# Performance work log

Measured on AMD Instinct MI355X. Metric: run time of the kernel, lower is better.

Reference implementation:

```python
import jax, jax.numpy as jnp
import numpy as np

N_NODES = 1024
CHANNELS = [1, 64, 128]
DENSE = [196608, 256]
SAMPLE_NUMBER = 50


def _glorot(key, shape):
    fan_in, fan_out = shape[0], shape[-1]
    s = jnp.sqrt(6.0 / (fan_in + fan_out))
    return jax.random.uniform(key, shape, jnp.float32, -s, s)


def setup_inputs() -> dict:
    key = jax.random.key(0)
    ks = jax.random.split(key, 20)
    T, B = 16, 64
    inp = {
        "xs_seq": jax.random.normal(ks[0], (T, B, N_NODES, CHANNELS[0]), jnp.float32),
        "adj": jax.random.uniform(ks[1], (N_NODES, N_NODES), jnp.float32) / N_NODES,
    }
    # GCGRU params per layer: gates z, r, candidate n over concat([x, h])
    ki = 2
    for li in range(len(CHANNELS) - 1):
        cin, cout = CHANNELS[li], CHANNELS[li + 1]
        for g in ("z", "r", "n"):
            inp[f"W{g}{li}"] = _glorot(ks[ki], (cin + cout, cout)); ki += 1
            inp[f"b{g}{li}"] = jnp.zeros((cout,), jnp.float32)
    inp["W_mu"] = _glorot(ks[ki], (DENSE[0], DENSE[1])); ki += 1
    inp["b_mu"] = jnp.zeros((DENSE[1],), jnp.float32)
    inp["W_lv"] = _glorot(ks[ki], (DENSE[0], DENSE[1])); ki += 1
    inp["b_lv"] = jnp.zeros((DENSE[1],), jnp.float32)
    return inp


def _gcgru(xs, adj, Wz, bz, Wr, br, Wn, bn, cout):
    # xs: [T, B, N, cin]; graph-conv GRU over time via scan
    T, B, N, _ = xs.shape
    h0 = jnp.zeros((B, N, cout), xs.dtype)

    def gconv(a, x, W, b):  # adj @ x @ W + b
        return jnp.einsum("ij,bjc,cd->bid", a, x, W) + b

    def step(h, x):
        xh = jnp.concatenate([x, h], axis=-1)
        z = jax.nn.sigmoid(gconv(adj, xh, Wz, bz))
        r = jax.nn.sigmoid(gconv(adj, xh, Wr, br))
        xrh = jnp.concatenate([x, r * h], axis=-1)
        n = jnp.tanh(gconv(adj, xrh, Wn, bn))
        h_new = (1.0 - z) * h + z * n
        return h_new, h_new

    _, hs = jax.lax.scan(step, h0, xs)
    return hs  # [T, B, N, cout]


def _forward(xs_seq, adj, Wz0, bz0, Wr0, br0, Wn0, bn0,
             Wz1, bz1, Wr1, br1, Wn1, bn1, W_mu, b_mu, W_lv, b_lv, eps):
    h1 = _gcgru(xs_seq, adj, Wz0, bz0, Wr0, br0, Wn0, bn0, CHANNELS[1])
    h2 = _gcgru(h1, adj, Wz1, bz1, Wr1, br1, Wn1, bn1, CHANNELS[2])
    xs = jnp.concatenate([h1[-1], h2[-1]], axis=2)  # [B, N, C1+C2]
    B = xs.shape[0]
    xs = xs.reshape(B, -1)  # [B, N*(C1+C2)]
    mu = jax.nn.sigmoid(xs @ W_mu + b_mu)
    logvar = jax.nn.sigmoid(xs @ W_lv + b_lv)
    std = jnp.exp(0.5 * logvar)
    z = mu + eps * std
    return z, mu, logvar


def reference(xs_seq, adj, Wz0, bz0, Wr0, br0, Wn0, bn0,
              Wz1, bz1, Wr1, br1, Wn1, bn1, W_mu, b_mu, W_lv, b_lv):
    B = xs_seq.shape[1]
    ekey = jax.random.fold_in(jax.random.key(0), 1234)
    eps = jax.random.normal(ekey, (SAMPLE_NUMBER, B, DENSE[1]), jnp.float32).mean(0)
    return _forward(xs_seq, adj, Wz0, bz0, Wr0, br0, Wn0, bn0,
                    Wz1, bz1, Wr1, br1, Wn1, bn1, W_mu, b_mu, W_lv, b_lv, eps)
```

## Files before the change

### kernel.cpp

```cpp
#include <hip/hip_runtime.h>
#include <math.h>

#define EPS_MODE 0

typedef unsigned short u16;
typedef short bf16x8 __attribute__((ext_vector_type(8)));
typedef float f32x4 __attribute__((ext_vector_type(4)));
typedef u16 u16x4 __attribute__((ext_vector_type(4)));
typedef u16 u16x8 __attribute__((ext_vector_type(8)));

static constexpr int T = 16;
static constexpr size_t MF = 1u << 20;
static constexpr int DKCH = 256;
static constexpr int DKCHUNK = 196608 / DKCH;

__device__ __forceinline__ u16 f2bf(float f) {
  unsigned u = __float_as_uint(f);
  unsigned r = (u + 0x7fffu + ((u >> 16) & 1u)) >> 16;
  return (u16)r;
}
__device__ __forceinline__ float bf2f(u16 h) {
  return __uint_as_float(((unsigned)h) << 16);
}
__device__ __forceinline__ void gload16(const void* g, void* l) {
  __builtin_amdgcn_global_load_lds(
      (const __attribute__((address_space(1))) void*)g,
      (__attribute__((address_space(3))) void*)l, 16, 0, 0);
}

__global__ __launch_bounds__(256) void cast_bf16(const float* __restrict__ in,
                                                 u16* __restrict__ out, int n) {
  int i = (blockIdx.x * 256 + threadIdx.x) * 4;
  if (i < n) {
    float4 v = *reinterpret_cast<const float4*>(&in[i]);
    out[i + 0] = f2bf(v.x); out[i + 1] = f2bf(v.y);
    out[i + 2] = f2bf(v.z); out[i + 3] = f2bf(v.w);
  }
}

__global__ __launch_bounds__(256) void prep_wt(const float* __restrict__ Wz0, const float* __restrict__ Wr0,
                                               const float* __restrict__ Wn0, const float* __restrict__ Wz1,
                                               const float* __restrict__ Wr1, const float* __restrict__ Wn1,
                                               u16* __restrict__ WzrT0, u16* __restrict__ WnT0,
                                               u16* __restrict__ WzrT1, u16* __restrict__ WnT1) {
  int seg = blockIdx.y;
  int idx = blockIdx.x * 256 + threadIdx.x;
  if (seg == 0) {
    if (idx < 128 * 64) {
      int j = idx >> 6, k = idx & 63;
      float v = (j < 64) ? Wz0[(k + 1) * 64 + j] : Wr0[(k + 1) * 64 + (j - 64)];
      WzrT0[idx] = f2bf(v);
    }
  } else if (seg == 1) {
    if (idx < 64 * 64) {
      int j = idx >> 6, k = idx & 63;
      WnT0[idx] = f2bf(Wn0[(k + 1) * 64 + j]);
    }
  } else if (seg == 2) {
    if (idx < 256 * 192) {
      int j = idx / 192, k = idx % 192;
      float v = (j < 128) ? Wz1[k * 128 + j] : Wr1[k * 128 + (j - 128)];
      WzrT1[idx] = f2bf(v);
    }
  } else {
    if (idx < 128 * 192) {
      int j = idx / 192, k = idx % 192;
      WnT1[idx] = f2bf(Wn1[k * 128 + j]);
    }
  }
}

template <int EPI, int LOGC, int MFR>
__global__ __launch_bounds__(256) void adj_mfma(const u16* __restrict__ A,
                                                const u16* __restrict__ BT,
                                                void* __restrict__ OUT) {
  constexpr int MT = MFR * 32;
  __shared__ __align__(16) char lds[(MFR + 4) * 4096];
  int tid = threadIdx.x;
  int w = tid >> 6, lane = tid & 63;
  int row0 = blockIdx.y * MT, col0 = blockIdx.x * 128;
  int wm = w >> 1, wn = w & 1;
  f32x4 acc[MFR][4] = {};
  for (int k0 = 0; k0 < 1024; k0 += 64) {
#pragma unroll
    for (int q = 0; q < MFR; ++q) {
      int row = q * 32 + w * 8 + (lane >> 3);
      gload16(A + (size_t)(row0 + row) * 1024 + k0 + (lane & 7) * 8,
              lds + q * 4096 + w * 1024);
    }
#pragma unroll
    for (int q = 0; q < 4; ++q) {
      int row = q * 32 + w * 8 + (lane >> 3);
      gload16(BT + (size_t)(col0 + row) * 1024 + k0 + (lane & 7) * 8,
              lds + MFR * 4096 + q * 4096 + w * 1024);
    }
    __syncthreads();
#pragma unroll
    for (int kk = 0; kk < 2; ++kk) {
      bf16x8 a[MFR], bb[4];
#pragma unroll
      for (int m = 0; m < MFR; ++m)
        a[m] = *(const bf16x8*)(lds + (wm * (MFR * 16) + m * 16 + (lane & 15)) * 128 + kk * 64 + (lane >> 4) * 16);
#pragma unroll
      for (int n = 0; n < 4; ++n)
        bb[n] = *(const bf16x8*)(lds + MFR * 4096 + (wn * 64 + n * 16 + (lane & 15)) * 128 + kk * 64 + (lane >> 4) * 16);
#pragma unroll
      for (int m = 0; m < MFR; ++m)
#pragma unroll
        for (int n = 0; n < 4; ++n)
          acc[m][n] = __builtin_amdgcn_mfma_f32_16x16x32_bf16(a[m], bb[n], acc[m][n], 0, 0, 0);
    }
    __syncthreads();
  }
  if (EPI == 1) {
    float* O = (float*)OUT;
#pragma unroll
    for (int m = 0; m < MFR; ++m)
#pragma unroll
      for (int n = 0; n < 4; ++n) {
        int col = col0 + wn * 64 + n * 16 + (lane & 15);
        int t = col >> 6, bbx = col & 63;
        int row = row0 + wm * (MFR * 16) + m * 16 + ((lane >> 4) << 2);
        *(float4*)&O[((size_t)t << 16) + ((size_t)bbx << 10) + row] = *(float4*)&acc[m][n];
      }
  } else {
    u16* O = (u16*)OUT;
    constexpr int C = 1 << LOGC;
#pragma unroll
    for (int m = 0; m < MFR; ++m)
#pragma unroll
      for (int n = 0; n < 4; ++n) {
        int col = col0 + wn * 64 + n * 16 + (lane & 15);
        int bbx = col >> LOGC, c = col & (C - 1);
#pragma unroll
        for (int j = 0; j < 4; ++j) {
          int row = row0 + wm * (MFR * 16) + m * 16 + ((lane >> 4) << 2) + j;
          O[(((size_t)bbx << 10) + row) * C + c] = f2bf(acc[m][n][j]);
        }
      }
  }
}

template <int C, int RK1, int MFR>
__global__ __launch_bounds__(256) void adj_ngate(
    const u16* __restrict__ A, const u16* __restrict__ BT,
    const u16* __restrict__ WnT, const float* __restrict__ bias,
    const float* __restrict__ axv, const float* __restrict__ wx,
    const u16* __restrict__ AH1, const u16* __restrict__ zT,
    u16* __restrict__ hT) {
  constexpr int LOGC = (C == 64) ? 6 : 7;
  constexpr int KW = (C == 64) ? 64 : 192;
  constexpr int KKAN = C / 32;
  constexpr int MT = MFR * 32;
  constexpr int STG = (MFR + 4) * 4096;
  constexpr int ANBYTES = MT * 136 * 2;
  constexpr int LDSZ = STG > ANBYTES ? STG : ANBYTES;
  __shared__ __align__(16) char lds[LDSZ];
  int tid = threadIdx.x;
  int w = tid >> 6, lane = tid & 63;
  int row0 = blockIdx.y * MT, col0 = blockIdx.x * 128;
  int wm = w >> 1, wn = w & 1;
  f32x4 acc[MFR][4] = {};
  for (int k0 = 0; k0 < 1024; k0 += 64) {
#pragma unroll
    for (int q = 0; q < MFR; ++q) {
      int row = q * 32 + w * 8 + (lane >> 3);
      gload16(A + (size_t)(row0 + row) * 1024 + k0 + (lane & 7) * 8,
              lds + q * 4096 + w * 1024);
    }
#pragma unroll
    for (int q = 0; q < 4; ++q) {
      int row = q * 32 + w * 8 + (lane >> 3);
      gload16(BT + (size_t)(col0 + row) * 1024 + k0 + (lane & 7) * 8,
              lds + MFR * 4096 + q * 4096 + w * 1024);
    }
    __syncthreads();
#pragma unroll
    for (int kk = 0; kk < 2; ++kk) {
      bf16x8 a[MFR], bb[4];
#pragma unroll
      for (int m = 0; m < MFR; ++m)
        a[m] = *(const bf16x8*)(lds + (wm * (MFR * 16) + m * 16 + (lane & 15)) * 128 + kk * 64 + (lane >> 4) * 16);
#pragma unroll
      for (int n = 0; n < 4; ++n)
        bb[n] = *(const bf16x8*)(lds + MFR * 4096 + (wn * 64 + n * 16 + (lane & 15)) * 128 + kk * 64 + (lane >> 4) * 16);
#pragma unroll
      for (int m = 0; m < MFR; ++m)
#pragma unroll
        for (int n = 0; n < 4; ++n)
          acc[m][n] = __builtin_amdgcn_mfma_f32_16x16x32_bf16(a[m], bb[n], acc[m][n], 0, 0, 0);
    }
    __syncthreads();
  }
  u16* ANt = (u16*)lds;
#pragma unroll
  for (int m = 0; m < MFR; ++m)
#pragma unroll
    for (int n = 0; n < 4; ++n) {
      int cl = wn * 64 + n * 16 + (lane & 15);
      int rl = wm * (MFR * 16) + m * 16 + ((lane >> 4) << 2);
#pragma unroll
      for (int j = 0; j < 4; ++j)
        ANt[(rl + j) * 136 + cl] = f2bf(acc[m][n][j]);
    }
  __syncthreads();
  int wrow = w >> 1, half = w & 1;
  int arow0 = wrow * (MFR * 16);
  int b0 = col0 >> LOGC;
  int out0 = (C == 64) ? 0 : half * 64;
  int kbase = (C == 64) ? half * 64 : 0;
  int b_eff = (C == 64) ? (b0 + half) : b0;
  constexpr int WOFF = (C == 64) ? 0 : 64;
  f32x4 acc2[MFR][4] = {};
#pragma unroll
  for (int kk = 0; kk < KKAN; ++kk) {
    bf16x8 a[MFR], bb[4];
    int ka = kbase + kk * 32 + (lane >> 4) * 8;
#pragma unroll
    for (int m = 0; m < MFR; ++m)
      a[m] = *(const bf16x8*)&ANt[(arow0 + m * 16 + (lane & 15)) * 136 + ka];
#pragma unroll
    for (int n = 0; n < 4; ++n)
      bb[n] = *(const bf16x8*)&WnT[(size_t)(out0 + n * 16 + (lane & 15)) * KW + WOFF + kk * 32 + (lane >> 4) * 8];
#pragma unroll
    for (int m = 0; m < MFR; ++m)
#pragma unroll
      for (int n = 0; n < 4; ++n)
        acc2[m][n] = __builtin_amdgcn_mfma_f32_16x16x32_bf16(a[m], bb[n], acc2[m][n], 0, 0, 0);
  }
  if (C == 128) {
#pragma unroll
    for (int kk = 0; kk < 2; ++kk) {
      bf16x8 a[MFR], bb[4];
#pragma unroll
      for (int m = 0; m < MFR; ++m)
        a[m] = *(const bf16x8*)&AH1[(((size_t)b0 << 10) + row0 + arow0 + m * 16 + (lane & 15)) * 64 + kk * 32 + (lane >> 4) * 8];
#pragma unroll
      for (int n = 0; n < 4; ++n)
        bb[n] = *(const bf16x8*)&WnT[(size_t)(out0 + n * 16 + (lane & 15)) * 192 + kk * 32 + (lane >> 4) * 8];
#pragma unroll
      for (int m = 0; m < MFR; ++m)
#pragma unroll
        for (int n = 0; n < 4; ++n)
          acc2[m][n] = __builtin_amdgcn_mfma_f32_16x16x32_bf16(a[m], bb[n], acc2[m][n], 0, 0, 0);
    }
  }
#pragma unroll
  for (int m = 0; m < MFR; ++m) {
    float ax4[4];
    if (RK1) {
      float4 v = *(const float4*)&axv[((size_t)b_eff << 10) + row0 + arow0 + m * 16 + ((lane >> 4) << 2)];
      ax4[0] = v.x; ax4[1] = v.y; ax4[2] = v.z; ax4[3] = v.w;
    }
#pragma unroll
    for (int n = 0; n < 4; ++n) {
      int cp = out0 + n * 16 + (lane & 15);
      int grow = arow0 + m * 16 + ((lane >> 4) << 2);
      size_t idx = (((size_t)b_eff << LOGC) + cp) * 1024 + row0 + grow;
      u16x4 zv = *(const u16x4*)&zT[idx];
      u16x4 hv = *(const u16x4*)&hT[idx];
      u16x4 pk;
#pragma unroll
      for (int j = 0; j < 4; ++j) {
        float g = acc2[m][n][j] + bias[cp];
        if (RK1) g += ax4[j] * wx[cp];
        float nv = tanhf(g);
        float z = bf2f(zv[j]), ho = bf2f(hv[j]);
        pk[j] = f2bf((1.f - z) * ho + z * nv);
      }
      *(u16x4*)&hT[idx] = pk;
    }
  }
}

template <int WM, int WN, int C, int NK1, int NK, int RK1>
__global__ __launch_bounds__(256) void gate_zr(
    const u16* __restrict__ A1, const u16* __restrict__ A2,
    const u16* __restrict__ WT, const float* __restrict__ bz,
    const float* __restrict__ br, const float* __restrict__ axv,
    const float* __restrict__ wxz, const float* __restrict__ wxr,
    const u16* __restrict__ hT, u16* __restrict__ zTo, u16* __restrict__ rhTo) {
  constexpr int MT = WM * 64, NT = WN * 64, K = NK * 64;
  constexpr int NB = 1024 / MT;
  __shared__ __align__(16) char lds[MT * 128 + NT * 128];
  int tid = threadIdx.x;
  int w = tid >> 6, lane = tid & 63;
  int by = blockIdx.x;
  int b = by / NB, n0 = (by % NB) * MT;
  size_t row0 = ((size_t)b << 10) + n0;
  int wm = w / WN, wn = w % WN;
  f32x4 acc[4][4] = {};
  for (int s = 0; s < NK; ++s) {
    const u16* As; int astr, koff;
    if (s < NK1) { As = A1; astr = 64; koff = s * 64; }
    else         { As = A2; astr = 128; koff = (s - NK1) * 64; }
#pragma unroll
    for (int q = 0; q < MT / 32; ++q) {
      int row = q * 32 + w * 8 + (lane >> 3);
      gload16(As + (row0 + row) * astr + koff + (lane & 7) * 8,
              lds + q * 4096 + w * 1024);
    }
#pragma unroll
    for (int q = 0; q < NT / 32; ++q) {
      int row = q * 32 + w * 8 + (lane >> 3);
      gload16(WT + (size_t)row * K + s * 64 + (lane & 7) * 8,
              lds + MT * 128 + q * 4096 + w * 1024);
    }
    __syncthreads();
#pragma unroll
    for (int kk = 0; kk < 2; ++kk) {
      bf16x8 a[4], bb[4];
#pragma unroll
      for (int m = 0; m < 4; ++m)
        a[m] = *(const bf16x8*)(lds + (wm * 64 + m * 16 + (lane & 15)) * 128 + kk * 64 + (lane >> 4) * 16);
#pragma unroll
      for (int n = 0; n < 4; ++n)
        bb[n] = *(const bf16x8*)(lds + MT * 128 + (wn * 64 + n * 16 + (lane & 15)) * 128 + kk * 64 + (lane >> 4) * 16);
#pragma unroll
      for (int m = 0; m < 4; ++m)
#pragma unroll
        for (int n = 0; n < 4; ++n)
          acc[m][n] = __builtin_amdgcn_mfma_f32_16x16x32_bf16(a[m], bb[n], acc[m][n], 0, 0, 0);
    }
    __syncthreads();
  }
#pragma unroll
  for (int m = 0; m < 4; ++m) {
    float ax4[4];
    if (RK1) {
      float4 v = *(const float4*)&axv[row0 + wm * 64 + m * 16 + ((lane >> 4) << 2)];
      ax4[0] = v.x; ax4[1] = v.y; ax4[2] = v.z; ax4[3] = v.w;
    }
#pragma unroll
    for (int n = 0; n < 4; ++n) {
      int cp = wn * 64 + n * 16 + (lane & 15);
      bool iz = cp < C;
      int c = iz ? cp : cp - C;
      int rl = wm * 64 + m * 16 + ((lane >> 4) << 2);
      size_t idx = (((size_t)b * C + c) << 10) + n0 + rl;
      u16x4 hv;
      if (!iz) hv = *(const u16x4*)&hT[idx];
      u16x4 pk;
#pragma unroll
      for (int j = 0; j < 4; ++j) {
        float g = acc[m][n][j] + (iz ? bz : br)[c];
        if (RK1) g += ax4[j] * (iz ? wxz : wxr)[c];
        float sg = 1.f / (1.f + expf(-g));
        pk[j] = iz ? f2bf(sg) : f2bf(sg * bf2f(hv[j]));
      }
      *(u16x4*)&(iz ? zTo : rhTo)[idx] = pk;
    }
  }
}

__global__ __launch_bounds__(256) void transpose_x(const u16* __restrict__ h1T,
                                                   const u16* __restrict__ h2T,
                                                   u16* __restrict__ X) {
  int b = blockIdx.x;
  int n0 = blockIdx.y * 128;
  __shared__ u16 tile[192][136];
  int tid = threadIdx.x;
#pragma unroll
  for (int i = 0; i < 12; ++i) {
    int id = tid + i * 256;
    int c = id >> 4, g = id & 15;
    u16x8 v;
    if (c < 64) v = *(const u16x8*)&h1T[(((size_t)b << 6) + c) * 1024 + n0 + g * 8];
    else        v = *(const u16x8*)&h2T[(((size_t)b << 7) + (c - 64)) * 1024 + n0 + g * 8];
    *(u16x8*)&tile[c][g * 8] = v;
  }
  __syncthreads();
#pragma unroll
  for (int i = 0; i < 12; ++i) {
    int id = tid + i * 256;
    int n = id / 24, g = id % 24;
    u16x8 v;
#pragma unroll
    for (int j = 0; j < 8; ++j) v[j] = tile[g * 8 + j][n];
    *(u16x8*)&X[(size_t)b * 196608 + (size_t)(n0 + n) * 192 + g * 8] = v;
  }
}

__global__ __launch_bounds__(256) void dense_split(const u16* __restrict__ X,
                                                   const float* __restrict__ Wmu,
                                                   const float* __restrict__ Wlv,
                                                   float* __restrict__ P) {
  int ot = blockIdx.x, ch = blockIdx.y, mat = blockIdx.z;
  const float* W = mat ? Wlv : Wmu;
  int o0 = ot * 64;
  __shared__ float As[16][68];
  __shared__ float Ws[16][68];
  int tid = threadIdx.x;
  int tx = tid & 15, ty = tid >> 4;
  int ab = tid >> 2, akq = (tid & 3) * 4;
  int wkk = tid >> 4, wo4 = (tid & 15) * 4;
  int kb = ch * DKCHUNK;
  float acc[4][4] = {};
  u16x4 xa = *(const u16x4*)&X[(size_t)ab * 196608 + kb + akq];
  float4 wv = *(const float4*)&W[(size_t)(kb + wkk) * 256 + o0 + wo4];
  for (int s = 0; s < DKCHUNK / 16; ++s) {
#pragma unroll
    for (int j = 0; j < 4; ++j) As[akq + j][ab] = bf2f(xa[j]);
    *(float4*)&Ws[wkk][wo4] = wv;
    __syncthreads();
    if (s + 1 < DKCHUNK / 16) {
      int k0 = kb + (s + 1) * 16;
      xa = *(const u16x4*)&X[(size_t)ab * 196608 + k0 + akq];
      wv = *(const float4*)&W[(size_t)(k0 + wkk) * 256 + o0 + wo4];
    }
#pragma unroll
    for (int kk = 0; kk < 16; ++kk) {
      float a[4], bq[4];
      *(float4*)a = *(const float4*)&As[kk][ty * 4];
      *(float4*)bq = *(const float4*)&Ws[kk][tx * 4];
#pragma unroll
      for (int i = 0; i < 4; ++i)
#pragma unroll
        for (int j = 0; j < 4; ++j) acc[i][j] += a[i] * bq[j];
    }
    __syncthreads();
  }
#pragma unroll
  for (int i = 0; i < 4; ++i) {
    float4 v; v.x = acc[i][0]; v.y = acc[i][1]; v.z = acc[i][2]; v.w = acc[i][3];
    *(float4*)&P[(((size_t)mat * DKCH + ch) * 64 + ty * 4 + i) * 256 + o0 + tx * 4] = v;
  }
}

__device__ __forceinline__ unsigned rotl32(unsigned v, int s) {
  return (v << s) | (v >> (32 - s));
}
__device__ void threefry(unsigned k0, unsigned k1, unsigned x0, unsigned x1,
                         unsigned& o0, unsigned& o1) {
  unsigned ks2 = k0 ^ k1 ^ 0x1BD11BDAu;
  unsigned a = x0 + k0, b = x1 + k1;
#define TF_RND(rot) { a += b; b = rotl32(b, rot); b ^= a; }
  TF_RND(13) TF_RND(15) TF_RND(26) TF_RND(6)
  a += k1; b += ks2 + 1u;
  TF_RND(17) TF_RND(29) TF_RND(16) TF_RND(24)
  a += ks2; b += k0 + 2u;
  TF_RND(13) TF_RND(15) TF_RND(26) TF_RND(6)
  a += k0; b += k1 + 3u;
  TF_RND(17) TF_RND(29) TF_RND(16) TF_RND(24)
  a += k1; b += ks2 + 4u;
  TF_RND(13) TF_RND(15) TF_RND(26) TF_RND(6)
  a += ks2; b += k0 + 5u;
#undef TF_RND
  o0 = a; o1 = b;
}

__device__ float u32_to_normal(unsigned bits) {
  unsigned fb = (bits >> 9) | 0x3F800000u;
  float f = __uint_as_float(fb) - 1.0f;
  const float lo = -0.99999994f;
  float u = f * 2.0f + lo;
  u = fmaxf(lo, u);
  float w = -log1pf(-u * u);
  float p;
  if (w < 5.0f) {
    w -= 2.5f;
    p = 2.81022636e-08f;
    p = fmaf(p, w, 3.43273939e-07f);
    p = fmaf(p, w, -3.5233877e-06f);
    p = fmaf(p, w, -4.39150654e-06f);
    p = fmaf(p, w, 0.00021858087f);
    p = fmaf(p, w, -0.00125372503f);
    p = fmaf(p, w, -0.00417768164f);
    p = fmaf(p, w, 0.246640727f);
    p = fmaf(p, w, 1.50140941f);
  } else {
    w = sqrtf(w) - 3.0f;
    p = -0.000200214257f;
    p = fmaf(p, w, 0.000100950558f);
    p = fmaf(p, w, 0.00134934322f);
    p = fmaf(p, w, -0.00367342844f);
    p = fmaf(p, w, 0.00573950773f);
    p = fmaf(p, w, -0.0076224613f);
    p = fmaf(p, w, 0.00943887047f);
    p = fmaf(p, w, 1.00167406f);
    p = fmaf(p, w, 2.83297682f);
  }
  return 1.41421354f * (p * u);
}

__global__ __launch_bounds__(256) void eps_kernel(float* __restrict__ eps) {
  int b = blockIdx.x;
  int o = threadIdx.x;
  unsigned k0, k1;
  threefry(0u, 0u, 0u, 1234u, k0, k1);
  float s = 0.f;
  for (int smp = 0; smp < 50; ++smp) {
    unsigned idx = ((unsigned)smp * 64u + (unsigned)b) * 256u + (unsigned)o;
    unsigned o0, o1, bits;
#if EPS_MODE == 0
    threefry(k0, k1, 0u, idx, o0, o1);
    bits = o0 ^ o1;
#else
    unsigned pp = idx % 409600u, half = idx / 409600u;
    threefry(k0, k1, pp, pp + 409600u, o0, o1);
    bits = half ? o1 : o0;
#endif
    s += u32_to_normal(bits);
  }
  eps[b * 256 + o] = s / 50.0f;
}

__global__ __launch_bounds__(256) void final_kernel(const float* __restrict__ P,
                                                    const float* __restrict__ bmu,
                                                    const float* __restrict__ blv,
                                                    const float* __restrict__ eps,
                                                    float* __restrict__ out) {
  int b = blockIdx.x, o = threadIdx.x;
  float smu = 0.f, slv = 0.f;
  for (int ch = 0; ch < DKCH; ++ch) {
    smu += P[(((size_t)0 * DKCH + ch) * 64 + b) * 256 + o];
    slv += P[(((size_t)1 * DKCH + ch) * 64 + b) * 256 + o];
  }
  float mu = 1.f / (1.f + expf(-(smu + bmu[o])));
  float lv = 1.f / (1.f + expf(-(slv + blv[o])));
  float z = mu + eps[b * 256 + o] * expf(0.5f * lv);
  out[b * 256 + o] = z;
  out[16384 + b * 256 + o] = mu;
  out[32768 + b * 256 + o] = lv;
}

extern "C" void kernel_launch(void* const* d_in, const int* in_sizes, int n_in,
                              void* d_out, int out_size, void* d_ws, size_t ws_size,
                              hipStream_t stream) {
  (void)in_sizes; (void)n_in; (void)out_size; (void)ws_size;
  const float* xs  = (const float*)d_in[0];
  const float* adj = (const float*)d_in[1];
  const float* Wz0 = (const float*)d_in[2];  const float* bz0 = (const float*)d_in[3];
  const float* Wr0 = (const float*)d_in[4];  const float* br0 = (const float*)d_in[5];
  const float* Wn0 = (const float*)d_in[6];  const float* bn0 = (const float*)d_in[7];
  const float* Wz1 = (const float*)d_in[8];  const float* bz1 = (const float*)d_in[9];
  const float* Wr1 = (const float*)d_in[10]; const float* br1 = (const float*)d_in[11];
  const float* Wn1 = (const float*)d_in[12]; const float* bn1 = (const float*)d_in[13];
  const float* Wmu = (const float*)d_in[14]; const float* bmu = (const float*)d_in[15];
  const float* Wlv = (const float*)d_in[16]; const float* blv = (const float*)d_in[17];

  float* ws = (float*)d_ws;
  u16*  adjB  = (u16*)(ws);
  u16*  xsB   = (u16*)(ws + MF / 2);
  float* AXv  = ws + 1 * MF;
  u16*  h1T   = (u16*)(ws + 2 * MF);
  u16*  h2T   = (u16*)(ws + 4 * MF);
  u16*  z0T   = (u16*)(ws + 8 * MF);
  u16*  z1T   = (u16*)(ws + 10 * MF);
  u16*  rh0T  = (u16*)(ws + 14 * MF);
  u16*  rh1T  = (u16*)(ws + 16 * MF);
  u16*  AH1   = (u16*)(ws + 20 * MF);
  u16*  AH2   = (u16*)(ws + 22 * MF);
  u16*  WTb   = (u16*)(ws + 26 * MF);
  u16*  X     = (u16*)(ws + 8 * MF);
  float* P    = ws + 16 * MF;
  float* EPS  = ws + 24 * MF;

  u16* WzrT0 = WTb;
  u16* WnT0  = WTb + 8192;
  u16* WzrT1 = WTb + 12288;
  u16* WnT1  = WTb + 61440;

  hipMemsetAsync(ws + 2 * MF, 0, 6 * MF * sizeof(float), stream);
  hipMemsetAsync(ws + 20 * MF, 0, 6 * MF * sizeof(float), stream);

  cast_bf16<<<1024, 256, 0, stream>>>(adj, adjB, 1 << 20);
  cast_bf16<<<1024, 256, 0, stream>>>(xs, xsB, 1 << 20);
  prep_wt<<<dim3(192, 4), 256, 0, stream>>>(Wz0, Wr0, Wn0, Wz1, Wr1, Wn1,
                                            WzrT0, WnT0, WzrT1, WnT1);

  adj_mfma<1, 0, 4><<<dim3(8, 8), 256, 0, stream>>>(adjB, xsB, AXv);

  for (int t = 0; t < T; ++t) {
    const float* AXt = AXv + (size_t)t * 65536;
    gate_zr<2, 2, 64, 1, 1, 1><<<512, 256, 0, stream>>>(
        AH1, nullptr, WzrT0, bz0, br0, AXt, Wz0, Wr0, h1T, z0T, rh0T);
    adj_ngate<64, 1, 2><<<dim3(32, 16), 256, 0, stream>>>(
        adjB, rh0T, WnT0, bn0, AXt, Wn0, nullptr, z0T, h1T);
    adj_mfma<0, 6, 2><<<dim3(32, 16), 256, 0, stream>>>(adjB, h1T, AH1);
    gate_zr<1, 4, 128, 1, 3, 0><<<1024, 256, 0, stream>>>(
        AH1, AH2, WzrT1, bz1, br1, nullptr, nullptr, nullptr, h2T, z1T, rh1T);
    adj_ngate<128, 0, 4><<<dim3(64, 8), 256, 0, stream>>>(
        adjB, rh1T, WnT1, bn1, nullptr, nullptr, AH1, z1T, h2T);
    if (t + 1 < T)
      adj_mfma<0, 7, 4><<<dim3(64, 8), 256, 0, stream>>>(adjB, h2T, AH2);
  }

  transpose_x<<<dim3(64, 8), 256, 0, stream>>>(h1T, h2T, X);
  dense_split<<<dim3(4, DKCH, 2), 256, 0, stream>>>(X, Wmu, Wlv, P);
  eps_kernel<<<64, 256, 0, stream>>>(EPS);
  final_kernel<<<64, 256, 0, stream>>>(P, bmu, blv, EPS, (float*)d_out);
}
```

Measured before the change: 3.025 ms.

## Skew GRU layers in time and fuse both layers' stages into combined kernels

Refactors the gate, n-gate and adjacency-matmul kernels into device functions. The time loop is then software-pipelined: layer-0 step t+1 runs in the same launch as layer-1 step t, through three combined kernels that dispatch by block index. This halves the number of launches per timestep and fills the GPU with more blocks per launch, to cut launch and tail-latency overhead in the serial recurrence. It also raises the layer-0 adjacency row tile from 2 to 4 MFMA fragments. It adds prologue and epilogue launches, and the combined kernels carry the larger shared-memory footprint of both branches, which may lower occupancy.

New measurement: 3.125 ms. 3.3% more time.

```diff
diff --git a/kernel.cpp b/kernel.cpp
--- a/kernel.cpp
+++ b/kernel.cpp
@@ -71,14 +71,14 @@
 }
 
 template <int EPI, int LOGC, int MFR>
-__global__ __launch_bounds__(256) void adj_mfma(const u16* __restrict__ A,
-                                                const u16* __restrict__ BT,
-                                                void* __restrict__ OUT) {
+__device__ __forceinline__ void dev_adj_mfma(int bx, int by, char* lds,
+                                             const u16* __restrict__ A,
+                                             const u16* __restrict__ BT,
+                                             void* __restrict__ OUT) {
   constexpr int MT = MFR * 32;
-  __shared__ __align__(16) char lds[(MFR + 4) * 4096];
   int tid = threadIdx.x;
   int w = tid >> 6, lane = tid & 63;
-  int row0 = blockIdx.y * MT, col0 = blockIdx.x * 128;
+  int row0 = by * MT, col0 = bx * 128;
   int wm = w >> 1, wn = w & 1;
   f32x4 acc[MFR][4] = {};
   for (int k0 = 0; k0 < 1024; k0 += 64) {
@@ -141,8 +141,17 @@
   }
 }
 
+template <int EPI, int LOGC, int MFR>
+__global__ __launch_bounds__(256) void adj_mfma(const u16* __restrict__ A,
+                                                const u16* __restrict__ BT,
+                                                void* __restrict__ OUT) {
+  __shared__ __align__(16) char lds[(MFR + 4) * 4096];
+  dev_adj_mfma<EPI, LOGC, MFR>(blockIdx.x, blockIdx.y, lds, A, BT, OUT);
+}
+
 template <int C, int RK1, int MFR>
-__global__ __launch_bounds__(256) void adj_ngate(
+__device__ __forceinline__ void dev_adj_ngate(
+    int bx, int by, char* lds,
     const u16* __restrict__ A, const u16* __restrict__ BT,
     const u16* __restrict__ WnT, const float* __restrict__ bias,
     const float* __restrict__ axv, const float* __restrict__ wx,
@@ -152,13 +161,9 @@
   constexpr int KW = (C == 64) ? 64 : 192;
   constexpr int KKAN = C / 32;
   constexpr int MT = MFR * 32;
-  constexpr int STG = (MFR + 4) * 4096;
-  constexpr int ANBYTES = MT * 136 * 2;
-  constexpr int LDSZ = STG > ANBYTES ? STG : ANBYTES;
-  __shared__ __align__(16) char lds[LDSZ];
   int tid = threadIdx.x;
   int w = tid >> 6, lane = tid & 63;
-  int row0 = blockIdx.y * MT, col0 = blockIdx.x * 128;
+  int row0 = by * MT, col0 = bx * 128;
   int wm = w >> 1, wn = w & 1;
   f32x4 acc[MFR][4] = {};
   for (int k0 = 0; k0 < 1024; k0 += 64) {
@@ -273,8 +278,25 @@
   }
 }
 
+template <int C, int RK1, int MFR>
+__global__ __launch_bounds__(256) void adj_ngate(
+    const u16* __restrict__ A, const u16* __restrict__ BT,
+    const u16* __restrict__ WnT, const float* __restrict__ bias,
+    const float* __restrict__ axv, const float* __restrict__ wx,
+    const u16* __restrict__ AH1, const u16* __restrict__ zT,
+    u16* __restrict__ hT) {
+  constexpr int MT = MFR * 32;
+  constexpr int STG = (MFR + 4) * 4096;
+  constexpr int ANB = MT * 136 * 2;
+  constexpr int LDSZ = STG > ANB ? STG : ANB;
+  __shared__ __align__(16) char lds[LDSZ];
+  dev_adj_ngate<C, RK1, MFR>(blockIdx.x, blockIdx.y, lds, A, BT, WnT, bias, axv, wx,
+                             AH1, zT, hT);
+}
+
 template <int WM, int WN, int C, int NK1, int NK, int RK1>
-__global__ __launch_bounds__(256) void gate_zr(
+__device__ __forceinline__ void dev_gate_zr(
+    int by, char* lds,
     const u16* __restrict__ A1, const u16* __restrict__ A2,
     const u16* __restrict__ WT, const float* __restrict__ bz,
     const float* __restrict__ br, const float* __restrict__ axv,
@@ -282,10 +304,8 @@
     const u16* __restrict__ hT, u16* __restrict__ zTo, u16* __restrict__ rhTo) {
   constexpr int MT = WM * 64, NT = WN * 64, K = NK * 64;
   constexpr int NB = 1024 / MT;
-  __shared__ __align__(16) char lds[MT * 128 + NT * 128];
   int tid = threadIdx.x;
   int w = tid >> 6, lane = tid & 63;
-  int by = blockIdx.x;
   int b = by / NB, n0 = (by % NB) * MT;
   size_t row0 = ((size_t)b << 10) + n0;
   int wm = w / WN, wn = w % WN;
@@ -350,6 +370,67 @@
       }
       *(u16x4*)&(iz ? zTo : rhTo)[idx] = pk;
     }
+  }
+}
+
+template <int WM, int WN, int C, int NK1, int NK, int RK1>
+__global__ __launch_bounds__(256) void gate_zr(
+    const u16* __restrict__ A1, const u16* __restrict__ A2,
+    const u16* __restrict__ WT, const float* __restrict__ bz,
+    const float* __restrict__ br, const float* __restrict__ axv,
+    const float* __restrict__ wxz, const float* __restrict__ wxr,
+    const u16* __restrict__ hT, u16* __restrict__ zTo, u16* __restrict__ rhTo) {
+  __shared__ __align__(16) char lds[WM * 64 * 128 + WN * 64 * 128];
+  dev_gate_zr<WM, WN, C, NK1, NK, RK1>(blockIdx.x, lds, A1, A2, WT, bz, br, axv,
+                                       wxz, wxr, hT, zTo, rhTo);
+}
+
+__global__ __launch_bounds__(256) void combo_zr(
+    const u16* __restrict__ AH1, const u16* __restrict__ AH2,
+    const u16* __restrict__ WzrT1, const float* __restrict__ bz1, const float* __restrict__ br1,
+    const u16* __restrict__ h2T, u16* __restrict__ z1T, u16* __restrict__ rh1T,
+    const u16* __restrict__ WzrT0, const float* __restrict__ bz0, const float* __restrict__ br0,
+    const float* __restrict__ AXt1, const float* __restrict__ Wz0, const float* __restrict__ Wr0,
+    const u16* __restrict__ h1T, u16* __restrict__ z0T, u16* __restrict__ rh0T) {
+  __shared__ __align__(16) char lds[40960];
+  int bid = blockIdx.x;
+  if (bid < 1024)
+    dev_gate_zr<1, 4, 128, 1, 3, 0>(bid, lds, AH1, AH2, WzrT1, bz1, br1, nullptr,
+                                    nullptr, nullptr, h2T, z1T, rh1T);
+  else
+    dev_gate_zr<2, 2, 64, 1, 1, 1>(bid - 1024, lds, AH1, nullptr, WzrT0, bz0, br0,
+                                   AXt1, Wz0, Wr0, h1T, z0T, rh0T);
+}
+
+__global__ __launch_bounds__(256) void combo_ngate(
+    const u16* __restrict__ adjB,
+    const u16* __restrict__ rh1T, const u16* __restrict__ WnT1, const float* __restrict__ bn1,
+    const u16* __restrict__ AH1, const u16* __restrict__ z1T, u16* __restrict__ h2T,
+    const u16* __restrict__ rh0T, const u16* __restrict__ WnT0, const float* __restrict__ bn0,
+    const float* __restrict__ AXt1, const float* __restrict__ Wn0,
+    const u16* __restrict__ z0T, u16* __restrict__ h1T) {
+  __shared__ __align__(16) char lds[34816];
+  int bid = blockIdx.x;
+  if (bid < 512)
+    dev_adj_ngate<128, 0, 4>(bid & 63, bid >> 6, lds, adjB, rh1T, WnT1, bn1,
+                             nullptr, nullptr, AH1, z1T, h2T);
+  else {
+    int b2 = bid - 512;
+    dev_adj_ngate<64, 1, 4>(b2 & 31, b2 >> 5, lds, adjB, rh0T, WnT0, bn0,
+                            AXt1, Wn0, nullptr, z0T, h1T);
+  }
+}
+
+__global__ __launch_bounds__(256) void combo_ah(
+    const u16* __restrict__ adjB, const u16* __restrict__ h2T, u16* __restrict__ AH2,
+    const u16* __restrict__ h1T, u16* __restrict__ AH1) {
+  __shared__ __align__(16) char lds[32768];
+  int bid = blockIdx.x;
+  if (bid < 512)
+    dev_adj_mfma<0, 7, 4>(bid & 63, bid >> 6, lds, adjB, h2T, AH2);
+  else {
+    int b2 = bid - 512;
+    dev_adj_mfma<0, 6, 4>(b2 & 31, b2 >> 5, lds, adjB, h1T, AH1);
   }
 }
 
@@ -571,20 +652,25 @@
 
   adj_mfma<1, 0, 4><<<dim3(8, 8), 256, 0, stream>>>(adjB, xsB, AXv);
 
-  for (int t = 0; t < T; ++t) {
-    const float* AXt = AXv + (size_t)t * 65536;
-    gate_zr<2, 2, 64, 1, 1, 1><<<512, 256, 0, stream>>>(
-        AH1, nullptr, WzrT0, bz0, br0, AXt, Wz0, Wr0, h1T, z0T, rh0T);
-    adj_ngate<64, 1, 2><<<dim3(32, 16), 256, 0, stream>>>(
-        adjB, rh0T, WnT0, bn0, AXt, Wn0, nullptr, z0T, h1T);
-    adj_mfma<0, 6, 2><<<dim3(32, 16), 256, 0, stream>>>(adjB, h1T, AH1);
-    gate_zr<1, 4, 128, 1, 3, 0><<<1024, 256, 0, stream>>>(
-        AH1, AH2, WzrT1, bz1, br1, nullptr, nullptr, nullptr, h2T, z1T, rh1T);
-    adj_ngate<128, 0, 4><<<dim3(64, 8), 256, 0, stream>>>(
-        adjB, rh1T, WnT1, bn1, nullptr, nullptr, AH1, z1T, h2T);
-    if (t + 1 < T)
-      adj_mfma<0, 7, 4><<<dim3(64, 8), 256, 0, stream>>>(adjB, h2T, AH2);
-  }
+  gate_zr<2, 2, 64, 1, 1, 1><<<512, 256, 0, stream>>>(
+      AH1, nullptr, WzrT0, bz0, br0, AXv, Wz0, Wr0, h1T, z0T, rh0T);
+  adj_ngate<64, 1, 4><<<dim3(32, 8), 256, 0, stream>>>(
+      adjB, rh0T, WnT0, bn0, AXv, Wn0, nullptr, z0T, h1T);
+  adj_mfma<0, 6, 4><<<dim3(32, 8), 256, 0, stream>>>(adjB, h1T, AH1);
+
+  for (int i = 0; i < T - 1; ++i) {
+    const float* AXt1 = AXv + (size_t)(i + 1) * 65536;
+    combo_zr<<<1536, 256, 0, stream>>>(AH1, AH2, WzrT1, bz1, br1, h2T, z1T, rh1T,
+                                       WzrT0, bz0, br0, AXt1, Wz0, Wr0, h1T, z0T, rh0T);
+    combo_ngate<<<768, 256, 0, stream>>>(adjB, rh1T, WnT1, bn1, AH1, z1T, h2T,
+                                         rh0T, WnT0, bn0, AXt1, Wn0, z0T, h1T);
+    combo_ah<<<768, 256, 0, stream>>>(adjB, h2T, AH2, h1T, AH1);
+  }
+
+  gate_zr<1, 4, 128, 1, 3, 0><<<1024, 256, 0, stream>>>(
+      AH1, AH2, WzrT1, bz1, br1, nullptr, nullptr, nullptr, h2T, z1T, rh1T);
+  adj_ngate<128, 0, 4><<<dim3(64, 8), 256, 0, stream>>>(
+      adjB, rh1T, WnT1, bn1, nullptr, nullptr, AH1, z1T, h2T);
 
   transpose_x<<<dim3(64, 8), 256, 0, stream>>>(h1T, h2T, X);
   dense_split<<<dim3(4, DKCH, 2), 256, 0, stream>>>(X, Wmu, Wlv, P);
```

## Rewrite dense split-K GEMM with bf16 MFMA and retune layer-2 adj kernels

Applied to the files above, without the earlier changes.

Replaces the scalar FP32 tiled dense projection with an MFMA bf16 kernel. Each block now covers all 256 outputs of one K chunk, staging X through LDS and converting W to bf16 on the fly. The FP32 weight stream (about 400MB across both matrices) still dominates, and converting W to bf16 reduces the precision of the product. Separately, the layer-2 adj_ngate and adj_mfma launches switch to a smaller per-block tile template argument with twice as many blocks.

Result: slower. 3.239 ms (+7.1%).

```diff
diff --git a/kernel.cpp b/kernel.cpp
--- a/kernel.cpp
+++ b/kernel.cpp
@@ -381,50 +381,72 @@
   }
 }
 
-__global__ __launch_bounds__(256) void dense_split(const u16* __restrict__ X,
+__global__ __launch_bounds__(256) void dense_mfma2(const u16* __restrict__ X,
                                                    const float* __restrict__ Wmu,
                                                    const float* __restrict__ Wlv,
                                                    float* __restrict__ P) {
-  int ot = blockIdx.x, ch = blockIdx.y, mat = blockIdx.z;
+  __shared__ __align__(16) char lds[8192 + 256 * 70 * 2];
+  u16* Bs = (u16*)(lds + 8192);
+  int tid = threadIdx.x, w = tid >> 6, lane = tid & 63;
+  int ch = blockIdx.x, mat = blockIdx.y;
   const float* W = mat ? Wlv : Wmu;
-  int o0 = ot * 64;
-  __shared__ float As[16][68];
-  __shared__ float Ws[16][68];
-  int tid = threadIdx.x;
-  int tx = tid & 15, ty = tid >> 4;
-  int ab = tid >> 2, akq = (tid & 3) * 4;
-  int wkk = tid >> 4, wo4 = (tid & 15) * 4;
   int kb = ch * DKCHUNK;
-  float acc[4][4] = {};
-  u16x4 xa = *(const u16x4*)&X[(size_t)ab * 196608 + kb + akq];
-  float4 wv = *(const float4*)&W[(size_t)(kb + wkk) * 256 + o0 + wo4];
-  for (int s = 0; s < DKCHUNK / 16; ++s) {
-#pragma unroll
-    for (int j = 0; j < 4; ++j) As[akq + j][ab] = bf2f(xa[j]);
-    *(float4*)&Ws[wkk][wo4] = wv;
-    __syncthreads();
-    if (s + 1 < DKCHUNK / 16) {
-      int k0 = kb + (s + 1) * 16;
-      xa = *(const u16x4*)&X[(size_t)ab * 196608 + k0 + akq];
-      wv = *(const float4*)&W[(size_t)(k0 + wkk) * 256 + o0 + wo4];
-    }
-#pragma unroll
-    for (int kk = 0; kk < 16; ++kk) {
-      float a[4], bq[4];
-      *(float4*)a = *(const float4*)&As[kk][ty * 4];
-      *(float4*)bq = *(const float4*)&Ws[kk][tx * 4];
-#pragma unroll
-      for (int i = 0; i < 4; ++i)
-#pragma unroll
-        for (int j = 0; j < 4; ++j) acc[i][j] += a[i] * bq[j];
-    }
-    __syncthreads();
-  }
-#pragma unroll
-  for (int i = 0; i < 4; ++i) {
-    float4 v; v.x = acc[i][0]; v.y = acc[i][1]; v.z = acc[i][2]; v.w = acc[i][3];
-    *(float4*)&P[(((size_t)mat * DKCH + ch) * 64 + ty * 4 + i) * 256 + o0 + tx * 4] = v;
-  }
+  int oL = tid & 63;
+  f32x4 acc[4][4] = {};
+  for (int s = 0; s < DKCHUNK / 64; ++s) {
+    int kg = kb + s * 64;
+#pragma unroll
+    for (int q = 0; q < 2; ++q) {
+      int row = q * 32 + w * 8 + (lane >> 3);
+      gload16(X + (size_t)row * 196608 + kg + (lane & 7) * 8,
+              lds + q * 4096 + w * 1024);
+    }
+#pragma unroll
+    for (int og = 0; og < 4; ++og) {
+      int o = og * 64 + oL;
+      float v[16];
+#pragma unroll
+      for (int kk = 0; kk < 16; ++kk)
+        v[kk] = W[(size_t)(kg + w * 16 + kk) * 256 + o];
+      u16x8 p0, p1;
+#pragma unroll
+      for (int j = 0; j < 8; ++j) p0[j] = f2bf(v[j]);
+#pragma unroll
+      for (int j = 0; j < 8; ++j) p1[j] = f2bf(v[8 + j]);
+      *(u16x8*)&Bs[o * 70 + w * 16] = p0;
+      *(u16x8*)&Bs[o * 70 + w * 16 + 8] = p1;
+    }
+    __syncthreads();
+#pragma unroll
+    for (int kk = 0; kk < 2; ++kk) {
+      bf16x8 a[4], bb[4];
+#pragma unroll
+      for (int m = 0; m < 4; ++m)
+        a[m] = *(const bf16x8*)(lds + (m * 16 + (lane & 15)) * 128 + kk * 64 + (lane >> 4) * 16);
+#pragma unroll
+      for (int n = 0; n < 4; ++n) {
+        int o = w * 64 + n * 16 + (lane & 15);
+        bb[n] = *(const bf16x8*)&Bs[o * 70 + kk * 32 + (lane >> 4) * 8];
+      }
+#pragma unroll
+      for (int m = 0; m < 4; ++m)
+#pragma unroll
+        for (int n = 0; n < 4; ++n)
+          acc[m][n] = __builtin_amdgcn_mfma_f32_16x16x32_bf16(a[m], bb[n], acc[m][n], 0, 0, 0);
+    }
+    __syncthreads();
+  }
+#pragma unroll
+  for (int m = 0; m < 4; ++m)
+#pragma unroll
+    for (int n = 0; n < 4; ++n) {
+      int o = w * 64 + n * 16 + (lane & 15);
+#pragma unroll
+      for (int j = 0; j < 4; ++j) {
+        int row = m * 16 + ((lane >> 4) << 2) + j;
+        P[(((size_t)mat * DKCH + ch) * 64 + row) * 256 + o] = acc[m][n][j];
+      }
+    }
 }
 
 __device__ __forceinline__ unsigned rotl32(unsigned v, int s) {
@@ -580,14 +602,14 @@
     adj_mfma<0, 6, 2><<<dim3(32, 16), 256, 0, stream>>>(adjB, h1T, AH1);
     gate_zr<1, 4, 128, 1, 3, 0><<<1024, 256, 0, stream>>>(
         AH1, AH2, WzrT1, bz1, br1, nullptr, nullptr, nullptr, h2T, z1T, rh1T);
-    adj_ngate<128, 0, 4><<<dim3(64, 8), 256, 0, stream>>>(
+    adj_ngate<128, 0, 2><<<dim3(64, 16), 256, 0, stream>>>(
         adjB, rh1T, WnT1, bn1, nullptr, nullptr, AH1, z1T, h2T);
     if (t + 1 < T)
-      adj_mfma<0, 7, 4><<<dim3(64, 8), 256, 0, stream>>>(adjB, h2T, AH2);
+      adj_mfma<0, 7, 2><<<dim3(64, 16), 256, 0, stream>>>(adjB, h2T, AH2);
   }
 
   transpose_x<<<dim3(64, 8), 256, 0, stream>>>(h1T, h2T, X);
-  dense_split<<<dim3(4, DKCH, 2), 256, 0, stream>>>(X, Wmu, Wlv, P);
+  dense_mfma2<<<dim3(DKCH, 2), 256, 0, stream>>>(X, Wmu, Wlv, P);
   eps_kernel<<<64, 256, 0, stream>>>(EPS);
   final_kernel<<<64, 256, 0, stream>>>(P, bmu, blv, EPS, (float*)d_out);
 }
```
